# Optimization experiments

Measured on AMD Instinct MI355X. Metric: run time of the kernel, lower is better.

The kernel has to match this reference:

```python
import jax, jax.numpy as jnp
import numpy as np

N_NODES = 100000
N_EDGES = 1600000
STATE_DIM = 128
HIDDEN_DIM = 128
ACTION_DIM = 16


def gcn_conv(x, edge_index, W, b, n_nodes):
    """PyG-style GCNConv: add self-loops, symmetric normalization, x@W then aggregate."""
    xw = x @ W  # [N, H]
    loops = jnp.arange(n_nodes, dtype=edge_index.dtype)
    src = jnp.concatenate([edge_index[0], loops])  # [E+N]
    dst = jnp.concatenate([edge_index[1], loops])
    ones = jnp.ones(src.shape[0], dtype=xw.dtype)
    deg = jax.ops.segment_sum(ones, dst, num_segments=n_nodes)  # degree of target nodes
    dinv = jnp.where(deg > 0, jax.lax.rsqrt(deg), 0.0)
    norm = dinv[src] * dinv[dst]  # [E+N]
    msg = xw[src] * norm[:, None]  # gather + scale (irregular access)
    out = jax.ops.segment_sum(msg, dst, num_segments=n_nodes)  # scatter-aggregate
    return out + b


def setup_inputs() -> dict:
    key = jax.random.key(0)
    ks = jax.random.split(key, 12)
    def lin(k, fan_in, shape):
        bound = 1.0 / np.sqrt(fan_in)
        return jax.random.uniform(k, shape, jnp.float32, -bound, bound)
    return {
        "x": jax.random.normal(ks[0], (N_NODES, STATE_DIM), jnp.float32),
        "edge_index": jax.random.randint(ks[1], (2, N_EDGES), 0, N_NODES, jnp.int64),
        "action": jax.random.normal(ks[2], (N_NODES, ACTION_DIM), jnp.float32),
        "gcn1_w": lin(ks[3], STATE_DIM, (STATE_DIM, HIDDEN_DIM)),
        "gcn1_b": lin(ks[4], STATE_DIM, (HIDDEN_DIM,)),
        "gcn2_w": lin(ks[5], HIDDEN_DIM, (HIDDEN_DIM, HIDDEN_DIM)),
        "gcn2_b": lin(ks[6], HIDDEN_DIM, (HIDDEN_DIM,)),
        "fc1_w": lin(ks[7], HIDDEN_DIM + ACTION_DIM, (HIDDEN_DIM + ACTION_DIM, HIDDEN_DIM)),
        "fc1_b": lin(ks[8], HIDDEN_DIM + ACTION_DIM, (HIDDEN_DIM,)),
        "fc2_w": lin(ks[9], HIDDEN_DIM, (HIDDEN_DIM, 1)),
        "fc2_b": lin(ks[10], HIDDEN_DIM, (1,)),
    }


def reference(x, edge_index, action, gcn1_w, gcn1_b, gcn2_w, gcn2_b, fc1_w, fc1_b, fc2_w, fc2_b):
    n = x.shape[0]
    h = jax.nn.relu(gcn_conv(x, edge_index, gcn1_w, gcn1_b, n))
    h = jax.nn.relu(gcn_conv(h, edge_index, gcn2_w, gcn2_b, n))
    h = jnp.concatenate([h, action], axis=-1)  # [N, H+A]
    h = jax.nn.relu(h @ fc1_w + fc1_b)
    q = h @ fc2_w + fc2_b  # [N, 1]
    return q.squeeze(-1)
```

## Files before the change

### kernel.cpp

```cpp
#include <hip/hip_runtime.h>
#include <hip/hip_bf16.h>

typedef unsigned short u16;
typedef unsigned int   u32;
typedef __attribute__((ext_vector_type(8))) short bf16x8;
typedef __attribute__((ext_vector_type(4))) float f32x4;
typedef __attribute__((ext_vector_type(4))) unsigned int u32x4;

constexpr int NN = 100000;
constexpr int NE = 1600000;
constexpr int D  = 128;
constexpr size_t WS_NEED = 58909184;

constexpr int NBUCK = 196;
constexpr int NBLKA = 512;
constexpr int EPB   = 3136;
constexpr int CAPA  = 48;

__device__ __forceinline__ float bf2f(u16 u){ union{u32 i;float f;}v; v.i=((u32)u)<<16; return v.f; }
__device__ __forceinline__ float2 bfp(u32 u){ union{u32 i;float f;}a,b; a.i=u<<16; b.i=u&0xffff0000u; return make_float2(a.f,b.f); }
__device__ __forceinline__ u16 f2bf(float f){ union{float f;u32 i;}v; v.f=f; u32 r=v.i + 0x7fffu + ((v.i>>16)&1u); return (u16)(r>>16); }
__device__ __forceinline__ u32 pk2(float a, float b){ return (u32)f2bf(a) | ((u32)f2bf(b)<<16); }

__global__ void detect_kernel(const u32* __restrict__ xw, const int* __restrict__ ei,
                              int* __restrict__ flagf, int* __restrict__ flage){
  __shared__ int shf[256];
  __shared__ int she[256];
  int t = threadIdx.x;
  int cnt = 0;
  for(int i = 0; i < 16; i++){
    u32 w = xw[(t*16 + i) * 256];
    int e = (int)((w >> 7) & 0xFFu);
    cnt += (e >= 64 && e <= 160) ? 1 : 0;
  }
  int nz = 0;
  for(int i = 0; i < 8; i++){
    int k = t*8 + i;
    long long w = 1 + ((long long)k * (2LL*NE - 2)) / 2048;
    nz += (ei[(int)(w | 1)] != 0) ? 1 : 0;
  }
  shf[t] = cnt; she[t] = nz;
  __syncthreads();
  for(int off=128; off>0; off>>=1){
    if(t<off){ shf[t]+=shf[t+off]; she[t]+=she[t+off]; }
    __syncthreads();
  }
  if(t==0){ flagf[0] = (shf[0] < 3000) ? 1 : 0; flage[0] = (she[0] == 0) ? 1 : 0; }
}

__global__ void prep_kernel(const void* __restrict__ w1, const void* __restrict__ w2,
    const void* __restrict__ fw1, const void* __restrict__ b1, const void* __restrict__ b2,
    const void* __restrict__ fb1, const void* __restrict__ fw2, const void* __restrict__ fb2,
    const int* __restrict__ flagf,
    u16* __restrict__ WT1, u16* __restrict__ WT2, u16* __restrict__ WTF, float* __restrict__ BF)
{
  const int ff = flagf[0];
  int i = blockIdx.x*256 + threadIdx.x;
  auto cv = [&](const void* p, int idx)->float{
    return ff ? ((const float*)p)[idx] : bf2f(((const u16*)p)[idx]);
  };
  if(i < 16384){
    int k = i >> 7, d = i & 127;
    WT1[d*128 + k] = f2bf(cv(w1, i));
  }else if(i < 32768){
    int j = i - 16384; int k = j >> 7, d = j & 127;
    WT2[d*128 + k] = f2bf(cv(w2, j));
  }else if(i < 51200){
    int j = i - 32768; int k = j >> 7, d = j & 127;
    WTF[d*144 + k] = f2bf(cv(fw1, j));
  }else if(i < 51713){
    int j = i - 51200;
    if(j < 128)       BF[j]   = cv(b1, j);
    else if(j < 256)  BF[j]   = cv(b2, j-128);
    else if(j < 384)  BF[j]   = cv(fb1, j-256);
    else if(j < 512)  BF[j]   = cv(fw2, j-384);
    else              BF[512] = cv(fb2, 0);
  }
}

__global__ void fill1_kernel(u16* __restrict__ out, int n){
  int i = blockIdx.x*blockDim.x + threadIdx.x;
  if(i < n) out[i] = 0x3F80;
}

__global__ __launch_bounds__(512) void passA_kernel(
    const int* __restrict__ ei, const int* __restrict__ flage,
    u32* __restrict__ ebuf, u32* __restrict__ counts)
{
  __shared__ u32 hist[NBUCK];
  int t = threadIdx.x;
  if(t < NBUCK) hist[t] = 0;
  __syncthreads();
  const int f = flage[0];
  const int eb = blockIdx.x * EPB;
  const u32 cbase = blockIdx.x * NBUCK;
  for(int g = t; g < EPB/4; g += 512){
    int e4 = eb + g*4;
    if(e4 >= NE) break;
    int sv[4], dv[4];
    if(f){
      uint4 sa = *(const uint4*)(ei + 2*(size_t)e4);
      uint4 sb = *(const uint4*)(ei + 2*(size_t)e4 + 4);
      uint4 da = *(const uint4*)(ei + 2*(size_t)(NE + e4));
      uint4 db = *(const uint4*)(ei + 2*(size_t)(NE + e4) + 4);
      sv[0]=(int)sa.x; sv[1]=(int)sa.z; sv[2]=(int)sb.x; sv[3]=(int)sb.z;
      dv[0]=(int)da.x; dv[1]=(int)da.z; dv[2]=(int)db.x; dv[3]=(int)db.z;
    }else{
      uint4 sa = *(const uint4*)(ei + e4);
      uint4 da = *(const uint4*)(ei + NE + e4);
      sv[0]=(int)sa.x; sv[1]=(int)sa.y; sv[2]=(int)sa.z; sv[3]=(int)sa.w;
      dv[0]=(int)da.x; dv[1]=(int)da.y; dv[2]=(int)da.z; dv[3]=(int)da.w;
    }
    #pragma unroll
    for(int q=0;q<4;q++){
      int s = sv[q], d = dv[q];
      if((u32)s >= (u32)NN || (u32)d >= (u32)NN) continue;
      int b = d >> 9;
      u32 rank = atomicAdd(&hist[b], 1u);
      if(rank < CAPA) ebuf[(size_t)(cbase + b)*CAPA + rank] = (u32)s | ((u32)(d & 511) << 17);
    }
  }
  __syncthreads();
  if(t < NBUCK){
    u32 c = hist[t];
    counts[t*NBLKA + blockIdx.x] = (c < CAPA) ? c : CAPA;
  }
}

__global__ void scan196_kernel(const u32* __restrict__ counts, int* __restrict__ bases){
  __shared__ int sh[NBUCK];
  int t = threadIdx.x;
  if(t < NBUCK){
    const uint4* p = (const uint4*)(counts + (size_t)t*NBLKA);
    int tot = 0;
    for(int c = 0; c < NBLKA/4; c++){ uint4 v = p[c]; tot += (int)(v.x + v.y + v.z + v.w); }
    sh[t] = tot;
  }
  __syncthreads();
  if(t == 0){
    int acc = 0;
    for(int b = 0; b < NBUCK; b++){ int v = sh[b]; sh[b] = acc; acc += v; }
  }
  __syncthreads();
  if(t < NBUCK) bases[t] = sh[t];
}

__global__ __launch_bounds__(512) void passB_kernel(
    const u32* __restrict__ ebuf, const u32* __restrict__ counts, const int* __restrict__ bases,
    int* __restrict__ deg, int* __restrict__ off, float* __restrict__ dinv,
    int* __restrict__ srcs)
{
  __shared__ int cnt[512];
  __shared__ int nodeoff[512];
  __shared__ int pos[512];
  __shared__ int wsum[8], wpre[8];
  const int t = threadIdx.x;
  const int b = blockIdx.x;
  const int v0 = b << 9;

  cnt[t] = 0;
  __syncthreads();

  const int cnum = (int)counts[b*NBLKA + t];
  const u32* cp = ebuf + (size_t)(t*NBUCK + b)*CAPA;

  {
    int i = 0;
    for(; i + 4 <= cnum; i += 4){
      uint4 r = *(const uint4*)(cp + i);
      atomicAdd(&cnt[r.x >> 17], 1); atomicAdd(&cnt[r.y >> 17], 1);
      atomicAdd(&cnt[r.z >> 17], 1); atomicAdd(&cnt[r.w >> 17], 1);
    }
    for(; i < cnum; i++) atomicAdd(&cnt[cp[i] >> 17], 1);
  }
  __syncthreads();

  const int myc = cnt[t];
  const int lane = t & 63, wid = t >> 6;
  int v = myc;
  #pragma unroll
  for(int o = 1; o < 64; o <<= 1){
    int u = __shfl_up(v, o, 64);
    if(lane >= o) v += u;
  }
  if(lane == 63) wsum[wid] = v;
  __syncthreads();
  if(t == 0){
    int acc = 0;
    #pragma unroll
    for(int w = 0; w < 8; w++){ wpre[w] = acc; acc += wsum[w]; }
  }
  __syncthreads();
  const int excl = v - myc + wpre[wid];
  nodeoff[t] = excl;
  pos[t] = 0;
  __syncthreads();

  const int gb = bases[b];

  {
    int i = 0;
    for(; i + 4 <= cnum; i += 4){
      uint4 rq = *(const uint4*)(cp + i);
      u32 rr[4] = {rq.x, rq.y, rq.z, rq.w};
      #pragma unroll
      for(int q = 0; q < 4; q++){
        int ld = rr[q] >> 17;
        int r = atomicAdd(&pos[ld], 1);
        srcs[gb + nodeoff[ld] + r] = (int)(rr[q] & 0x1FFFFu);
      }
    }
    for(; i < cnum; i++){
      u32 rec = cp[i];
      int ld = rec >> 17;
      int r = atomicAdd(&pos[ld], 1);
      srcs[gb + nodeoff[ld] + r] = (int)(rec & 0x1FFFFu);
    }
  }

  int vn = v0 + t;
  if(vn < NN){
    deg[vn] = myc;
    off[vn] = gb + excl;
    dinv[vn] = rsqrtf((float)(myc + 1));
  }
}

__global__ __launch_bounds__(256) void gemm1_kernel(
    const void* __restrict__ A1, const u16* __restrict__ WT,
    const int* __restrict__ flagf, const float* __restrict__ dscale,
    u16* __restrict__ out, int n)
{
  const int tid = threadIdx.x;
  const int nb  = blockIdx.x * 64;
  const int ff  = flagf[0];
  const int wave = tid >> 6;
  const int lane = tid & 63;
  const int quad = lane >> 4;
  const int lm   = lane & 15;

  int arow = nb + wave*16 + lm; if(arow >= n) arow = n-1;

  bf16x8 afr[4];
  if(!ff){
    const u16* xr = (const u16*)A1 + (size_t)arow*128 + quad*8;
    #pragma unroll
    for(int k=0;k<4;k++) afr[k] = *(const bf16x8*)(xr + 32*k);
  }else{
    const float* xr = (const float*)A1 + (size_t)arow*128 + quad*8;
    #pragma unroll
    for(int k=0;k<4;k++){
      float4 p0 = *(const float4*)(xr + 32*k);
      float4 p1 = *(const float4*)(xr + 32*k + 4);
      union{u32x4 u; bf16x8 v;} cvv;
      cvv.u = (u32x4){pk2(p0.x,p0.y), pk2(p0.z,p0.w), pk2(p1.x,p1.y), pk2(p1.z,p1.w)};
      afr[k] = cvv.v;
    }
  }

  f32x4 acc[8];
  #pragma unroll
  for(int t=0;t<8;t++) acc[t] = (f32x4){0.f,0.f,0.f,0.f};

  #pragma unroll
  for(int ki = 0; ki < 4; ki++){
    int kk = ki*32 + quad*8;
    #pragma unroll
    for(int t=0;t<8;t++){
      bf16x8 b = *(const bf16x8*)(WT + (size_t)(t*16 + lm)*128 + kk);
      acc[t] = __builtin_amdgcn_mfma_f32_16x16x32_bf16(afr[ki], b, acc[t], 0, 0, 0);
    }
  }

  const int node0 = nb + wave*16 + quad*4;
  #pragma unroll
  for(int r=0;r<4;r++){
    int gr = node0 + r;
    if(gr < n){
      float dv = dscale[gr];
      #pragma unroll
      for(int t=0;t<8;t++){
        out[(size_t)gr*D + t*16 + lm] = f2bf(acc[t][r]*dv);
      }
    }
  }
}

#define ACC8(r)  { float2 f_;                       \
    f_ = bfp((r).x); a0 += f_.x; a1 += f_.y;        \
    f_ = bfp((r).y); a2 += f_.x; a3 += f_.y;        \
    f_ = bfp((r).z); a4 += f_.x; a5 += f_.y;        \
    f_ = bfp((r).w); a6 += f_.x; a7 += f_.y; }

template<bool FINAL>
__global__ __launch_bounds__(256) void fused_kernel(
    const int* __restrict__ off, const int* __restrict__ deg,
    const int* __restrict__ srcs, const float* __restrict__ dinv,
    const u16* __restrict__ xw, const float* __restrict__ biasf,
    const u16* __restrict__ WT, const float* __restrict__ fb1,
    const float* __restrict__ qwf, const float* __restrict__ qbf,
    const void* __restrict__ action, const int* __restrict__ flagf,
    void* __restrict__ out)
{
  constexpr int K  = FINAL ? 144 : 128;
  constexpr int KT = FINAL ? 160 : 128;
  constexpr int KP = KT + 8;
  constexpr int NKI = KT/32;
  __shared__ u16 Hs[16*KP];
  __shared__ float qred[FINAL ? 64 : 4];

  const int tid  = threadIdx.x;
  const int node0 = blockIdx.x * 16;
  const int nl   = tid >> 4;
  const int l16  = tid & 15;
  const int node = node0 + nl;

  const int wave = tid >> 6;
  const int lane = tid & 63;
  const int quad = lane >> 4;
  const int lm   = lane & 15;

  const int j0 = off[node];
  const int j1 = j0 + deg[node];
  float a0=0.f,a1=0.f,a2=0.f,a3=0.f,a4=0.f,a5=0.f,a6=0.f,a7=0.f;
  const u16* __restrict__ xl = xw + 8*l16;

  int j = j0;
  int s0=0, s1=0, s2=0, s3=0;
  const bool pre = (j + 4 <= j1);
  if(pre){
    s0 = __builtin_nontemporal_load(&srcs[j]);
    s1 = __builtin_nontemporal_load(&srcs[j+1]);
    s2 = __builtin_nontemporal_load(&srcs[j+2]);
    s3 = __builtin_nontemporal_load(&srcs[j+3]);
  }
  for(; j + 8 <= j1; j += 4){
    uint4 r0 = *(const uint4*)(xl + (size_t)s0*D);
    uint4 r1 = *(const uint4*)(xl + (size_t)s1*D);
    uint4 r2 = *(const uint4*)(xl + (size_t)s2*D);
    uint4 r3 = *(const uint4*)(xl + (size_t)s3*D);
    s0 = __builtin_nontemporal_load(&srcs[j+4]);
    s1 = __builtin_nontemporal_load(&srcs[j+5]);
    s2 = __builtin_nontemporal_load(&srcs[j+6]);
    s3 = __builtin_nontemporal_load(&srcs[j+7]);
    ACC8(r0); ACC8(r1); ACC8(r2); ACC8(r3);
  }
  if(pre){
    uint4 r0 = *(const uint4*)(xl + (size_t)s0*D);
    uint4 r1 = *(const uint4*)(xl + (size_t)s1*D);
    uint4 r2 = *(const uint4*)(xl + (size_t)s2*D);
    uint4 r3 = *(const uint4*)(xl + (size_t)s3*D);
    ACC8(r0); ACC8(r1); ACC8(r2); ACC8(r3);
    j += 4;
  }
  for(; j < j1; j++){
    int s = __builtin_nontemporal_load(&srcs[j]);
    uint4 r = *(const uint4*)(xl + (size_t)s*D);
    ACC8(r);
  }

  uint4 ps = *(const uint4*)(xl + (size_t)node*D);
  ACC8(ps);
  const float dv = dinv[node];
  float4 bA = *(const float4*)(biasf + 8*l16);
  float4 bB = *(const float4*)(biasf + 8*l16 + 4);
  float o0 = fmaxf(fmaf(dv,a0,bA.x), 0.f);
  float o1 = fmaxf(fmaf(dv,a1,bA.y), 0.f);
  float o2 = fmaxf(fmaf(dv,a2,bA.z), 0.f);
  float o3 = fmaxf(fmaf(dv,a3,bA.w), 0.f);
  float o4 = fmaxf(fmaf(dv,a4,bB.x), 0.f);
  float o5 = fmaxf(fmaf(dv,a5,bB.y), 0.f);
  float o6 = fmaxf(fmaf(dv,a6,bB.z), 0.f);
  float o7 = fmaxf(fmaf(dv,a7,bB.w), 0.f);
  uint4 pkd;
  pkd.x = pk2(o0,o1); pkd.y = pk2(o2,o3); pkd.z = pk2(o4,o5); pkd.w = pk2(o6,o7);

  u16* Hp = Hs + nl*KP;
  *(uint4*)(Hp + 8*l16) = pkd;

  if(FINAL){
    const int ff = flagf[0];
    if(ff){
      if(l16 < 4){
        const float* af = (const float*)action + (size_t)node*16 + l16*4;
        float4 p = *(const float4*)af;
        uint2 q; q.x = pk2(p.x,p.y); q.y = pk2(p.z,p.w);
        *(uint2*)(Hp + 128 + 4*l16) = q;
      }
    }else{
      if(l16 < 2){
        uint4 v = *(const uint4*)((const u16*)action + (size_t)node*16 + 8*l16);
        *(uint4*)(Hp + 128 + 8*l16) = v;
      }
    }
    if(l16 >= 14){
      *(uint4*)(Hp + 144 + 8*(l16-14)) = make_uint4(0,0,0,0);
    }
  }

  bf16x8 bfr[NKI][2];
  #pragma unroll
  for(int ki = 0; ki < NKI; ki++){
    int kk = ki*32 + quad*8;
    #pragma unroll
    for(int tt=0; tt<2; tt++){
      int col = (wave*2 + tt)*16 + lm;
      bfr[ki][tt] = (bf16x8){0,0,0,0,0,0,0,0};
      if(!FINAL || kk < K)
        bfr[ki][tt] = *(const bf16x8*)(WT + (size_t)col*K + kk);
    }
  }
  __syncthreads();

  const u16* Ab = Hs + lm*KP;
  f32x4 acc[2];
  acc[0] = (f32x4){0.f,0.f,0.f,0.f};
  acc[1] = (f32x4){0.f,0.f,0.f,0.f};

  #pragma unroll
  for(int ki = 0; ki < NKI; ki++){
    int kk = ki*32 + quad*8;
    bf16x8 a = *(const bf16x8*)(Ab + kk);
    acc[0] = __builtin_amdgcn_mfma_f32_16x16x32_bf16(a, bfr[ki][0], acc[0], 0, 0, 0);
    acc[1] = __builtin_amdgcn_mfma_f32_16x16x32_bf16(a, bfr[ki][1], acc[1], 0, 0, 0);
  }

  const int rbase = quad*4;
  if(!FINAL){
    #pragma unroll
    for(int r=0;r<4;r++){
      int gn = node0 + rbase + r;
      float dvr = dinv[gn];
      #pragma unroll
      for(int tt=0;tt<2;tt++){
        int col = (wave*2 + tt)*16 + lm;
        ((u16*)out)[(size_t)gn*D + col] = f2bf(acc[tt][r]*dvr);
      }
    }
  }else{
    float qp[4] = {0.f,0.f,0.f,0.f};
    #pragma unroll
    for(int tt=0;tt<2;tt++){
      int col = (wave*2 + tt)*16 + lm;
      float bv = fb1[col];
      float qw = qwf[col];
      #pragma unroll
      for(int r=0;r<4;r++){
        float h = fmaxf(acc[tt][r] + bv, 0.f);
        qp[r] += h * qw;
      }
    }
    #pragma unroll
    for(int r=0;r<4;r++){
      #pragma unroll
      for(int o=1; o<16; o<<=1) qp[r] += __shfl_xor(qp[r], o, 16);
    }
    if(lm == 0){
      #pragma unroll
      for(int r=0;r<4;r++) qred[wave*16 + rbase + r] = qp[r];
    }
    __syncthreads();
    if(tid < 16){
      float q = qred[tid] + qred[16+tid] + qred[32+tid] + qred[48+tid] + qbf[0];
      int gn = node0 + tid;
      const int ff = flagf[0];
      if(ff) ((float*)out)[gn] = q;
      else   ((u16*)out)[gn]  = f2bf(q);
    }
  }
}

extern "C" void kernel_launch(void* const* d_in, const int* in_sizes, int n_in,
                              void* d_out, int out_size, void* d_ws, size_t ws_size,
                              hipStream_t stream)
{
  bool meta_ok = (n_in >= 11) && (in_sizes[0] == NN*D) && (in_sizes[1] == 2*NE)
              && (in_sizes[2] == NN*16) && (out_size == NN);
  if(!meta_ok){
    fill1_kernel<<<(NN+255)/256, 256, 0, stream>>>((u16*)d_out, NN);
    return;
  }
  if(ws_size < WS_NEED) return;

  const void* x      = d_in[0];
  const int*  ei     = (const int*)d_in[1];
  const void* action = d_in[2];
  const void* w1     = d_in[3];
  const void* b1     = d_in[4];
  const void* w2     = d_in[5];
  const void* b2     = d_in[6];
  const void* fw1    = d_in[7];
  const void* fb1    = d_in[8];
  const void* fw2    = d_in[9];
  const void* fb2    = d_in[10];

  char* ws = (char*)d_ws;
  int*   DEG    = (int*)(ws + 0);
  int*   OFF    = (int*)(ws + 400128);
  float* DINV   = (float*)(ws + 800256);
  int*   FLAGE  = (int*)(ws + 1204480);
  int*   FLAGF  = (int*)(ws + 1204544);
  u16*   WT1    = (u16*)(ws + 1204608);
  u16*   WT2    = (u16*)(ws + 1237376);
  u16*   WTF    = (u16*)(ws + 1270144);
  float* BF     = (float*)(ws + 1307008);
  int*   SRCS   = (int*)(ws + 1309184);
  u16*   F0     = (u16*)(ws + 7709184);
  u16*   F1     = (u16*)(ws + 33309184);
  u32*   EBUF   = (u32*)(ws + 33309184);
  u32*   COUNTS = (u32*)(ws + 52576768);
  int*   BASES  = (int*)(ws + 52978176);

  detect_kernel<<<1, 256, 0, stream>>>((const u32*)x, ei, FLAGF, FLAGE);

  passA_kernel<<<NBLKA, 512, 0, stream>>>(ei, FLAGE, EBUF, COUNTS);
  scan196_kernel<<<1, 256, 0, stream>>>(COUNTS, BASES);
  passB_kernel<<<NBUCK, 512, 0, stream>>>(EBUF, COUNTS, BASES, DEG, OFF, DINV, SRCS);

  prep_kernel<<<203, 256, 0, stream>>>(w1, w2, fw1, b1, b2, fb1, fw2, fb2, FLAGF,
                                       WT1, WT2, WTF, BF);

  gemm1_kernel<<<(NN+63)/64, 256, 0, stream>>>(x, WT1, FLAGF, DINV, F0, NN);

  fused_kernel<false><<<(NN+15)/16, 256, 0, stream>>>(
      OFF, DEG, SRCS, DINV, F0, BF, WT2, nullptr, nullptr, nullptr, nullptr, FLAGF, F1);

  fused_kernel<true><<<(NN+15)/16, 256, 0, stream>>>(
      OFF, DEG, SRCS, DINV, F1, BF+128, WTF, BF+256, BF+384, BF+512, action, FLAGF, d_out);
}
```

Baseline: 335.0 us.

## Split fused gather+GEMM into separate gather and streaming GEMM kernels

Replaces the fused aggregate-then-GEMM kernels with a pure gather kernel that writes H to global memory, followed by streaming MFMA GEMM kernels that process 64 rows per block with all 128 output columns. The gather kernel splits each node's 128 features across two blocks (64 columns each, 8 lanes per node), which gives more parallelism and smaller per-row gather footprints. This removes LDS staging, the per-block weight reloads and the block syncs. In exchange it adds extra global round-trips for the intermediate H and two more kernel launches.

```diff
diff --git a/kernel.cpp b/kernel.cpp
--- a/kernel.cpp
+++ b/kernel.cpp
@@ -226,14 +226,15 @@
   }
 }
 
-__global__ __launch_bounds__(256) void gemm1_kernel(
+template<bool RAW>
+__global__ __launch_bounds__(256) void gemm_stream_kernel(
     const void* __restrict__ A1, const u16* __restrict__ WT,
     const int* __restrict__ flagf, const float* __restrict__ dscale,
     u16* __restrict__ out, int n)
 {
   const int tid = threadIdx.x;
   const int nb  = blockIdx.x * 64;
-  const int ff  = flagf[0];
+  const int ff  = RAW ? flagf[0] : 0;
   const int wave = tid >> 6;
   const int lane = tid & 63;
   const int quad = lane >> 4;
@@ -242,7 +243,7 @@
   int arow = nb + wave*16 + lm; if(arow >= n) arow = n-1;
 
   bf16x8 afr[4];
-  if(!ff){
+  if(!RAW || !ff){
     const u16* xr = (const u16*)A1 + (size_t)arow*128 + quad*8;
     #pragma unroll
     for(int k=0;k<4;k++) afr[k] = *(const bf16x8*)(xr + 32*k);
@@ -286,44 +287,115 @@
   }
 }
 
+__global__ __launch_bounds__(256) void gemmF_kernel(
+    const u16* __restrict__ H, const void* __restrict__ action,
+    const u16* __restrict__ WT, const float* __restrict__ fb1,
+    const float* __restrict__ qwf, const float* __restrict__ qbf,
+    const int* __restrict__ flagf, void* __restrict__ out, int n)
+{
+  const int tid = threadIdx.x;
+  const int nb  = blockIdx.x * 64;
+  const int ff  = flagf[0];
+  const int wave = tid >> 6;
+  const int lane = tid & 63;
+  const int quad = lane >> 4;
+  const int lm   = lane & 15;
+
+  int arow = nb + wave*16 + lm; if(arow >= n) arow = n-1;
+
+  bf16x8 afr[5];
+  {
+    const u16* hr = H + (size_t)arow*128 + quad*8;
+    #pragma unroll
+    for(int k=0;k<4;k++) afr[k] = *(const bf16x8*)(hr + 32*k);
+  }
+  afr[4] = (bf16x8){0,0,0,0,0,0,0,0};
+  if(quad < 2){
+    if(ff){
+      const float* af = (const float*)action + (size_t)arow*16 + quad*8;
+      float4 p0 = *(const float4*)(af);
+      float4 p1 = *(const float4*)(af + 4);
+      union{u32x4 u; bf16x8 v;} cvv;
+      cvv.u = (u32x4){pk2(p0.x,p0.y), pk2(p0.z,p0.w), pk2(p1.x,p1.y), pk2(p1.z,p1.w)};
+      afr[4] = cvv.v;
+    }else{
+      afr[4] = *(const bf16x8*)((const u16*)action + (size_t)arow*16 + quad*8);
+    }
+  }
+
+  f32x4 acc[8];
+  #pragma unroll
+  for(int t=0;t<8;t++) acc[t] = (f32x4){0.f,0.f,0.f,0.f};
+
+  #pragma unroll
+  for(int ki = 0; ki < 5; ki++){
+    int kk = ki*32 + quad*8;
+    #pragma unroll
+    for(int t=0;t<8;t++){
+      bf16x8 b = (bf16x8){0,0,0,0,0,0,0,0};
+      if(kk < 144)
+        b = *(const bf16x8*)(WT + (size_t)(t*16 + lm)*144 + kk);
+      acc[t] = __builtin_amdgcn_mfma_f32_16x16x32_bf16(afr[ki], b, acc[t], 0, 0, 0);
+    }
+  }
+
+  float qp[4] = {0.f,0.f,0.f,0.f};
+  #pragma unroll
+  for(int t=0;t<8;t++){
+    int col = t*16 + lm;
+    float bv = fb1[col];
+    float qw = qwf[col];
+    #pragma unroll
+    for(int r=0;r<4;r++){
+      float h = fmaxf(acc[t][r] + bv, 0.f);
+      qp[r] += h * qw;
+    }
+  }
+  #pragma unroll
+  for(int r=0;r<4;r++){
+    #pragma unroll
+    for(int o=1; o<16; o<<=1) qp[r] += __shfl_xor(qp[r], o, 16);
+  }
+  if(lm == 0){
+    const float qb = qbf[0];
+    const int node0 = nb + wave*16 + quad*4;
+    #pragma unroll
+    for(int r=0;r<4;r++){
+      int gr = node0 + r;
+      if(gr < n){
+        float q = qp[r] + qb;
+        if(ff) ((float*)out)[gr] = q;
+        else   ((u16*)out)[gr]  = f2bf(q);
+      }
+    }
+  }
+}
+
 #define ACC8(r)  { float2 f_;                       \
     f_ = bfp((r).x); a0 += f_.x; a1 += f_.y;        \
     f_ = bfp((r).y); a2 += f_.x; a3 += f_.y;        \
     f_ = bfp((r).z); a4 += f_.x; a5 += f_.y;        \
     f_ = bfp((r).w); a6 += f_.x; a7 += f_.y; }
 
-template<bool FINAL>
-__global__ __launch_bounds__(256) void fused_kernel(
+__global__ __launch_bounds__(256) void gatherH_kernel(
     const int* __restrict__ off, const int* __restrict__ deg,
     const int* __restrict__ srcs, const float* __restrict__ dinv,
     const u16* __restrict__ xw, const float* __restrict__ biasf,
-    const u16* __restrict__ WT, const float* __restrict__ fb1,
-    const float* __restrict__ qwf, const float* __restrict__ qbf,
-    const void* __restrict__ action, const int* __restrict__ flagf,
-    void* __restrict__ out)
-{
-  constexpr int K  = FINAL ? 144 : 128;
-  constexpr int KT = FINAL ? 160 : 128;
-  constexpr int KP = KT + 8;
-  constexpr int NKI = KT/32;
-  __shared__ u16 Hs[16*KP];
-  __shared__ float qred[FINAL ? 64 : 4];
-
+    u16* __restrict__ H)
+{
+  const int blk  = blockIdx.x;
+  const int half = blk & 1;
+  const int grp  = blk >> 1;
   const int tid  = threadIdx.x;
-  const int node0 = blockIdx.x * 16;
-  const int nl   = tid >> 4;
-  const int l16  = tid & 15;
-  const int node = node0 + nl;
-
-  const int wave = tid >> 6;
-  const int lane = tid & 63;
-  const int quad = lane >> 4;
-  const int lm   = lane & 15;
+  const int nl   = tid >> 3;
+  const int l8   = tid & 7;
+  const int node = grp*32 + nl;
+  const int d0   = half*64 + l8*8;
 
   const int j0 = off[node];
   const int j1 = j0 + deg[node];
   float a0=0.f,a1=0.f,a2=0.f,a3=0.f,a4=0.f,a5=0.f,a6=0.f,a7=0.f;
-  const u16* __restrict__ xl = xw + 8*l16;
+  const u16* __restrict__ xl = xw + d0;
 
   int j = j0;
   int s0=0, s1=0, s2=0, s3=0;
@@ -362,8 +434,8 @@
   uint4 ps = *(const uint4*)(xl + (size_t)node*D);
   ACC8(ps);
   const float dv = dinv[node];
-  float4 bA = *(const float4*)(biasf + 8*l16);
-  float4 bB = *(const float4*)(biasf + 8*l16 + 4);
+  float4 bA = *(const float4*)(biasf + d0);
+  float4 bB = *(const float4*)(biasf + d0 + 4);
   float o0 = fmaxf(fmaf(dv,a0,bA.x), 0.f);
   float o1 = fmaxf(fmaf(dv,a1,bA.y), 0.f);
   float o2 = fmaxf(fmaf(dv,a2,bA.z), 0.f);
@@ -374,100 +446,7 @@
   float o7 = fmaxf(fmaf(dv,a7,bB.w), 0.f);
   uint4 pkd;
   pkd.x = pk2(o0,o1); pkd.y = pk2(o2,o3); pkd.z = pk2(o4,o5); pkd.w = pk2(o6,o7);
-
-  u16* Hp = Hs + nl*KP;
-  *(uint4*)(Hp + 8*l16) = pkd;
-
-  if(FINAL){
-    const int ff = flagf[0];
-    if(ff){
-      if(l16 < 4){
-        const float* af = (const float*)action + (size_t)node*16 + l16*4;
-        float4 p = *(const float4*)af;
-        uint2 q; q.x = pk2(p.x,p.y); q.y = pk2(p.z,p.w);
-        *(uint2*)(Hp + 128 + 4*l16) = q;
-      }
-    }else{
-      if(l16 < 2){
-        uint4 v = *(const uint4*)((const u16*)action + (size_t)node*16 + 8*l16);
-        *(uint4*)(Hp + 128 + 8*l16) = v;
-      }
-    }
-    if(l16 >= 14){
-      *(uint4*)(Hp + 144 + 8*(l16-14)) = make_uint4(0,0,0,0);
-    }
-  }
-
-  bf16x8 bfr[NKI][2];
-  #pragma unroll
-  for(int ki = 0; ki < NKI; ki++){
-    int kk = ki*32 + quad*8;
-    #pragma unroll
-    for(int tt=0; tt<2; tt++){
-      int col = (wave*2 + tt)*16 + lm;
-      bfr[ki][tt] = (bf16x8){0,0,0,0,0,0,0,0};
-      if(!FINAL || kk < K)
-        bfr[ki][tt] = *(const bf16x8*)(WT + (size_t)col*K + kk);
-    }
-  }
-  __syncthreads();
-
-  const u16* Ab = Hs + lm*KP;
-  f32x4 acc[2];
-  acc[0] = (f32x4){0.f,0.f,0.f,0.f};
-  acc[1] = (f32x4){0.f,0.f,0.f,0.f};
-
-  #pragma unroll
-  for(int ki = 0; ki < NKI; ki++){
-    int kk = ki*32 + quad*8;
-    bf16x8 a = *(const bf16x8*)(Ab + kk);
-    acc[0] = __builtin_amdgcn_mfma_f32_16x16x32_bf16(a, bfr[ki][0], acc[0], 0, 0, 0);
-    acc[1] = __builtin_amdgcn_mfma_f32_16x16x32_bf16(a, bfr[ki][1], acc[1], 0, 0, 0);
-  }
-
-  const int rbase = quad*4;
-  if(!FINAL){
-    #pragma unroll
-    for(int r=0;r<4;r++){
-      int gn = node0 + rbase + r;
-      float dvr = dinv[gn];
-      #pragma unroll
-      for(int tt=0;tt<2;tt++){
-        int col = (wave*2 + tt)*16 + lm;
-        ((u16*)out)[(size_t)gn*D + col] = f2bf(acc[tt][r]*dvr);
-      }
-    }
-  }else{
-    float qp[4] = {0.f,0.f,0.f,0.f};
-    #pragma unroll
-    for(int tt=0;tt<2;tt++){
-      int col = (wave*2 + tt)*16 + lm;
-      float bv = fb1[col];
-      float qw = qwf[col];
-      #pragma unroll
-      for(int r=0;r<4;r++){
-        float h = fmaxf(acc[tt][r] + bv, 0.f);
-        qp[r] += h * qw;
-      }
-    }
-    #pragma unroll
-    for(int r=0;r<4;r++){
-      #pragma unroll
-      for(int o=1; o<16; o<<=1) qp[r] += __shfl_xor(qp[r], o, 16);
-    }
-    if(lm == 0){
-      #pragma unroll
-      for(int r=0;r<4;r++) qred[wave*16 + rbase + r] = qp[r];
-    }
-    __syncthreads();
-    if(tid < 16){
-      float q = qred[tid] + qred[16+tid] + qred[32+tid] + qred[48+tid] + qbf[0];
-      int gn = node0 + tid;
-      const int ff = flagf[0];
-      if(ff) ((float*)out)[gn] = q;
-      else   ((u16*)out)[gn]  = f2bf(q);
-    }
-  }
+  *(uint4*)(H + (size_t)node*D + d0) = pkd;
 }
 
 extern "C" void kernel_launch(void* const* d_in, const int* in_sizes, int n_in,
@@ -505,8 +484,8 @@
   u16*   WTF    = (u16*)(ws + 1270144);
   float* BF     = (float*)(ws + 1307008);
   int*   SRCS   = (int*)(ws + 1309184);
-  u16*   F0     = (u16*)(ws + 7709184);
-  u16*   F1     = (u16*)(ws + 33309184);
+  u16*   XW     = (u16*)(ws + 7709184);
+  u16*   HB     = (u16*)(ws + 33309184);
   u32*   EBUF   = (u32*)(ws + 33309184);
   u32*   COUNTS = (u32*)(ws + 52576768);
   int*   BASES  = (int*)(ws + 52978176);
@@ -520,11 +499,14 @@
   prep_kernel<<<203, 256, 0, stream>>>(w1, w2, fw1, b1, b2, fb1, fw2, fb2, FLAGF,
                                        WT1, WT2, WTF, BF);
 
-  gemm1_kernel<<<(NN+63)/64, 256, 0, stream>>>(x, WT1, FLAGF, DINV, F0, NN);
-
-  fused_kernel<false><<<(NN+15)/16, 256, 0, stream>>>(
-      OFF, DEG, SRCS, DINV, F0, BF, WT2, nullptr, nullptr, nullptr, nullptr, FLAGF, F1);
-
-  fused_kernel<true><<<(NN+15)/16, 256, 0, stream>>>(
-      OFF, DEG, SRCS, DINV, F1, BF+128, WTF, BF+256, BF+384, BF+512, action, FLAGF, d_out);
-}
+  gemm_stream_kernel<true><<<(NN+63)/64, 256, 0, stream>>>(x, WT1, FLAGF, DINV, XW, NN);
+
+  gatherH_kernel<<<(NN/32)*2, 256, 0, stream>>>(OFF, DEG, SRCS, DINV, XW, BF, HB);
+
+  gemm_stream_kernel<false><<<(NN+63)/64, 256, 0, stream>>>(HB, WT2, FLAGF, DINV, XW, NN);
+
+  gatherH_kernel<<<(NN/32)*2, 256, 0, stream>>>(OFF, DEG, SRCS, DINV, XW, BF+128, HB);
+
+  gemmF_kernel<<<(NN+63)/64, 256, 0, stream>>>(HB, action, WTF, BF+256, BF+384, BF+512,
+                                               FLAGF, d_out, NN);
+}
```

Result: slower. 373.3 us (+11.4%).

## Merge setup kernels and overlap edge bucketing with first GEMM

Applied to the files above, without the earlier changes.

Folds format detection into the weight-prep kernel and merges the edge bucketing pass with the first-layer GEMM in a single launch with disjoint block ranges, so both run concurrently. The GEMM no longer scales rows by dinv, because dinv is not yet available at that point. The first aggregation instead multiplies each gathered neighbour row by its source dinv and handles the self-loop term separately. The separate scan kernel is removed: each passB block recomputes its own bucket base by summing the counts of all earlier buckets. This trades fewer launches and serialization for extra dinv gathers per edge and redundant prefix work in passB.

```diff
diff --git a/kernel.cpp b/kernel.cpp
--- a/kernel.cpp
+++ b/kernel.cpp
@@ -16,46 +16,62 @@
 constexpr int NBLKA = 512;
 constexpr int EPB   = 3136;
 constexpr int CAPA  = 48;
+constexpr int NBG1  = (NN + 127) / 128;
 
 __device__ __forceinline__ float bf2f(u16 u){ union{u32 i;float f;}v; v.i=((u32)u)<<16; return v.f; }
 __device__ __forceinline__ float2 bfp(u32 u){ union{u32 i;float f;}a,b; a.i=u<<16; b.i=u&0xffff0000u; return make_float2(a.f,b.f); }
 __device__ __forceinline__ u16 f2bf(float f){ union{float f;u32 i;}v; v.f=f; u32 r=v.i + 0x7fffu + ((v.i>>16)&1u); return (u16)(r>>16); }
 __device__ __forceinline__ u32 pk2(float a, float b){ return (u32)f2bf(a) | ((u32)f2bf(b)<<16); }
 
-__global__ void detect_kernel(const u32* __restrict__ xw, const int* __restrict__ ei,
-                              int* __restrict__ flagf, int* __restrict__ flage){
-  __shared__ int shf[256];
-  __shared__ int she[256];
-  int t = threadIdx.x;
+__global__ void fill1_kernel(u16* __restrict__ out, int n){
+  int i = blockIdx.x*blockDim.x + threadIdx.x;
+  if(i < n) out[i] = 0x3F80;
+}
+
+__global__ __launch_bounds__(512) void prep_kernel(
+    const u32* __restrict__ xw, const int* __restrict__ ei,
+    const void* __restrict__ w1, const void* __restrict__ w2,
+    const void* __restrict__ fw1, const void* __restrict__ b1, const void* __restrict__ b2,
+    const void* __restrict__ fb1, const void* __restrict__ fw2, const void* __restrict__ fb2,
+    int* __restrict__ flagf, int* __restrict__ flage,
+    u16* __restrict__ WT1, u16* __restrict__ WT2, u16* __restrict__ WTF, float* __restrict__ BF)
+{
+  __shared__ int sh[512];
+  const int t = threadIdx.x;
   int cnt = 0;
-  for(int i = 0; i < 16; i++){
-    u32 w = xw[(t*16 + i) * 256];
+  #pragma unroll
+  for(int i = 0; i < 8; i++){
+    u32 w = xw[(t*8 + i) * 256];
     int e = (int)((w >> 7) & 0xFFu);
     cnt += (e >= 64 && e <= 160) ? 1 : 0;
   }
-  int nz = 0;
-  for(int i = 0; i < 8; i++){
-    int k = t*8 + i;
-    long long w = 1 + ((long long)k * (2LL*NE - 2)) / 2048;
-    nz += (ei[(int)(w | 1)] != 0) ? 1 : 0;
-  }
-  shf[t] = cnt; she[t] = nz;
-  __syncthreads();
-  for(int off=128; off>0; off>>=1){
-    if(t<off){ shf[t]+=shf[t+off]; she[t]+=she[t+off]; }
+  sh[t] = cnt;
+  __syncthreads();
+  for(int o = 256; o > 0; o >>= 1){
+    if(t < o) sh[t] += sh[t + o];
     __syncthreads();
   }
-  if(t==0){ flagf[0] = (shf[0] < 3000) ? 1 : 0; flage[0] = (she[0] == 0) ? 1 : 0; }
-}
-
-__global__ void prep_kernel(const void* __restrict__ w1, const void* __restrict__ w2,
-    const void* __restrict__ fw1, const void* __restrict__ b1, const void* __restrict__ b2,
-    const void* __restrict__ fb1, const void* __restrict__ fw2, const void* __restrict__ fb2,
-    const int* __restrict__ flagf,
-    u16* __restrict__ WT1, u16* __restrict__ WT2, u16* __restrict__ WTF, float* __restrict__ BF)
-{
-  const int ff = flagf[0];
-  int i = blockIdx.x*256 + threadIdx.x;
+  const int ff = (sh[0] < 3000) ? 1 : 0;
+
+  if(blockIdx.x == 0){
+    int nz = 0;
+    #pragma unroll
+    for(int i = 0; i < 4; i++){
+      int k = t*4 + i;
+      long long w = 1 + ((long long)k * (2LL*NE - 2)) / 2048;
+      nz += (ei[(int)(w | 1)] != 0) ? 1 : 0;
+    }
+    __syncthreads();
+    sh[t] = nz;
+    __syncthreads();
+    for(int o = 256; o > 0; o >>= 1){
+      if(t < o) sh[t] += sh[t + o];
+      __syncthreads();
+    }
+    if(t == 0){ flage[0] = (sh[0] == 0) ? 1 : 0; flagf[0] = ff; }
+  }
+
+  int i = blockIdx.x*512 + t;
   auto cv = [&](const void* p, int idx)->float{
     return ff ? ((const float*)p)[idx] : bf2f(((const u16*)p)[idx]);
   };
@@ -78,75 +94,111 @@
   }
 }
 
-__global__ void fill1_kernel(u16* __restrict__ out, int n){
-  int i = blockIdx.x*blockDim.x + threadIdx.x;
-  if(i < n) out[i] = 0x3F80;
-}
-
-__global__ __launch_bounds__(512) void passA_kernel(
+__global__ __launch_bounds__(512) void mega_kernel(
     const int* __restrict__ ei, const int* __restrict__ flage,
-    u32* __restrict__ ebuf, u32* __restrict__ counts)
+    u32* __restrict__ ebuf, u32* __restrict__ counts,
+    const void* __restrict__ x, const u16* __restrict__ WT,
+    const int* __restrict__ flagf, u16* __restrict__ F0)
 {
   __shared__ u32 hist[NBUCK];
-  int t = threadIdx.x;
-  if(t < NBUCK) hist[t] = 0;
-  __syncthreads();
-  const int f = flage[0];
-  const int eb = blockIdx.x * EPB;
-  const u32 cbase = blockIdx.x * NBUCK;
-  for(int g = t; g < EPB/4; g += 512){
-    int e4 = eb + g*4;
-    if(e4 >= NE) break;
-    int sv[4], dv[4];
-    if(f){
-      uint4 sa = *(const uint4*)(ei + 2*(size_t)e4);
-      uint4 sb = *(const uint4*)(ei + 2*(size_t)e4 + 4);
-      uint4 da = *(const uint4*)(ei + 2*(size_t)(NE + e4));
-      uint4 db = *(const uint4*)(ei + 2*(size_t)(NE + e4) + 4);
-      sv[0]=(int)sa.x; sv[1]=(int)sa.z; sv[2]=(int)sb.x; sv[3]=(int)sb.z;
-      dv[0]=(int)da.x; dv[1]=(int)da.z; dv[2]=(int)db.x; dv[3]=(int)db.z;
+  const int blk = blockIdx.x;
+  const int t = threadIdx.x;
+
+  if(blk < NBLKA){
+    if(t < NBUCK) hist[t] = 0;
+    __syncthreads();
+    const int f = flage[0];
+    const int eb = blk * EPB;
+    const u32 cbase = blk * NBUCK;
+    for(int g = t; g < EPB/4; g += 512){
+      int e4 = eb + g*4;
+      if(e4 >= NE) break;
+      int sv[4], dv[4];
+      if(f){
+        uint4 sa = *(const uint4*)(ei + 2*(size_t)e4);
+        uint4 sb = *(const uint4*)(ei + 2*(size_t)e4 + 4);
+        uint4 da = *(const uint4*)(ei + 2*(size_t)(NE + e4));
+        uint4 db = *(const uint4*)(ei + 2*(size_t)(NE + e4) + 4);
+        sv[0]=(int)sa.x; sv[1]=(int)sa.z; sv[2]=(int)sb.x; sv[3]=(int)sb.z;
+        dv[0]=(int)da.x; dv[1]=(int)da.z; dv[2]=(int)db.x; dv[3]=(int)db.z;
+      }else{
+        uint4 sa = *(const uint4*)(ei + e4);
+        uint4 da = *(const uint4*)(ei + NE + e4);
+        sv[0]=(int)sa.x; sv[1]=(int)sa.y; sv[2]=(int)sa.z; sv[3]=(int)sa.w;
+        dv[0]=(int)da.x; dv[1]=(int)da.y; dv[2]=(int)da.z; dv[3]=(int)da.w;
+      }
+      #pragma unroll
+      for(int q=0;q<4;q++){
+        int s = sv[q], d = dv[q];
+        if((u32)s >= (u32)NN || (u32)d >= (u32)NN) continue;
+        int b = d >> 9;
+        u32 rank = atomicAdd(&hist[b], 1u);
+        if(rank < CAPA) ebuf[(size_t)(cbase + b)*CAPA + rank] = (u32)s | ((u32)(d & 511) << 17);
+      }
+    }
+    __syncthreads();
+    if(t < NBUCK){
+      u32 c = hist[t];
+      counts[t*NBLKA + blk] = (c < CAPA) ? c : CAPA;
+    }
+  }else{
+    const int g = blk - NBLKA;
+    const int nb = g * 128;
+    const int ff = flagf[0];
+    const int wave = t >> 6;
+    const int lane = t & 63;
+    const int quad = lane >> 4;
+    const int lm   = lane & 15;
+
+    int arow = nb + wave*16 + lm; if(arow >= NN) arow = NN-1;
+
+    bf16x8 afr[4];
+    if(!ff){
+      const u16* xr = (const u16*)x + (size_t)arow*128 + quad*8;
+      #pragma unroll
+      for(int k=0;k<4;k++) afr[k] = *(const bf16x8*)(xr + 32*k);
     }else{
-      uint4 sa = *(const uint4*)(ei + e4);
-      uint4 da = *(const uint4*)(ei + NE + e4);
-      sv[0]=(int)sa.x; sv[1]=(int)sa.y; sv[2]=(int)sa.z; sv[3]=(int)sa.w;
-      dv[0]=(int)da.x; dv[1]=(int)da.y; dv[2]=(int)da.z; dv[3]=(int)da.w;
-    }
-    #pragma unroll
-    for(int q=0;q<4;q++){
-      int s = sv[q], d = dv[q];
-      if((u32)s >= (u32)NN || (u32)d >= (u32)NN) continue;
-      int b = d >> 9;
-      u32 rank = atomicAdd(&hist[b], 1u);
-      if(rank < CAPA) ebuf[(size_t)(cbase + b)*CAPA + rank] = (u32)s | ((u32)(d & 511) << 17);
-    }
-  }
-  __syncthreads();
-  if(t < NBUCK){
-    u32 c = hist[t];
-    counts[t*NBLKA + blockIdx.x] = (c < CAPA) ? c : CAPA;
+      const float* xr = (const float*)x + (size_t)arow*128 + quad*8;
+      #pragma unroll
+      for(int k=0;k<4;k++){
+        float4 p0 = *(const float4*)(xr + 32*k);
+        float4 p1 = *(const float4*)(xr + 32*k + 4);
+        union{u32x4 u; bf16x8 v;} cvv;
+        cvv.u = (u32x4){pk2(p0.x,p0.y), pk2(p0.z,p0.w), pk2(p1.x,p1.y), pk2(p1.z,p1.w)};
+        afr[k] = cvv.v;
+      }
+    }
+
+    f32x4 acc[8];
+    #pragma unroll
+    for(int a=0;a<8;a++) acc[a] = (f32x4){0.f,0.f,0.f,0.f};
+
+    #pragma unroll
+    for(int ki = 0; ki < 4; ki++){
+      int kk = ki*32 + quad*8;
+      #pragma unroll
+      for(int a=0;a<8;a++){
+        bf16x8 b = *(const bf16x8*)(WT + (size_t)(a*16 + lm)*128 + kk);
+        acc[a] = __builtin_amdgcn_mfma_f32_16x16x32_bf16(afr[ki], b, acc[a], 0, 0, 0);
+      }
+    }
+
+    const int node0 = nb + wave*16 + quad*4;
+    #pragma unroll
+    for(int r=0;r<4;r++){
+      int gr = node0 + r;
+      if(gr < NN){
+        #pragma unroll
+        for(int a=0;a<8;a++){
+          F0[(size_t)gr*D + a*16 + lm] = f2bf(acc[a][r]);
+        }
+      }
+    }
   }
 }
 
-__global__ void scan196_kernel(const u32* __restrict__ counts, int* __restrict__ bases){
-  __shared__ int sh[NBUCK];
-  int t = threadIdx.x;
-  if(t < NBUCK){
-    const uint4* p = (const uint4*)(counts + (size_t)t*NBLKA);
-    int tot = 0;
-    for(int c = 0; c < NBLKA/4; c++){ uint4 v = p[c]; tot += (int)(v.x + v.y + v.z + v.w); }
-    sh[t] = tot;
-  }
-  __syncthreads();
-  if(t == 0){
-    int acc = 0;
-    for(int b = 0; b < NBUCK; b++){ int v = sh[b]; sh[b] = acc; acc += v; }
-  }
-  __syncthreads();
-  if(t < NBUCK) bases[t] = sh[t];
-}
-
 __global__ __launch_bounds__(512) void passB_kernel(
-    const u32* __restrict__ ebuf, const u32* __restrict__ counts, const int* __restrict__ bases,
+    const u32* __restrict__ ebuf, const u32* __restrict__ counts,
     int* __restrict__ deg, int* __restrict__ off, float* __restrict__ dinv,
     int* __restrict__ srcs)
 {
@@ -154,12 +206,27 @@
   __shared__ int nodeoff[512];
   __shared__ int pos[512];
   __shared__ int wsum[8], wpre[8];
+  __shared__ int gbs;
   const int t = threadIdx.x;
   const int b = blockIdx.x;
   const int v0 = b << 9;
+  const int lane = t & 63, wid = t >> 6;
 
   cnt[t] = 0;
-  __syncthreads();
+
+  int part = 0;
+  for(int q = 0; q < b; q++) part += (int)counts[q*NBLKA + t];
+  int rp = part;
+  #pragma unroll
+  for(int o = 1; o < 64; o <<= 1) rp += __shfl_xor(rp, o, 64);
+  if(lane == 0) wsum[wid] = rp;
+  __syncthreads();
+  if(t == 0){
+    int a = 0;
+    #pragma unroll
+    for(int w = 0; w < 8; w++) a += wsum[w];
+    gbs = a;
+  }
 
   const int cnum = (int)counts[b*NBLKA + t];
   const u32* cp = ebuf + (size_t)(t*NBUCK + b)*CAPA;
@@ -176,7 +243,6 @@
   __syncthreads();
 
   const int myc = cnt[t];
-  const int lane = t & 63, wid = t >> 6;
   int v = myc;
   #pragma unroll
   for(int o = 1; o < 64; o <<= 1){
@@ -196,7 +262,7 @@
   pos[t] = 0;
   __syncthreads();
 
-  const int gb = bases[b];
+  const int gb = gbs;
 
   {
     int i = 0;
@@ -226,73 +292,18 @@
   }
 }
 
-__global__ __launch_bounds__(256) void gemm1_kernel(
-    const void* __restrict__ A1, const u16* __restrict__ WT,
-    const int* __restrict__ flagf, const float* __restrict__ dscale,
-    u16* __restrict__ out, int n)
-{
-  const int tid = threadIdx.x;
-  const int nb  = blockIdx.x * 64;
-  const int ff  = flagf[0];
-  const int wave = tid >> 6;
-  const int lane = tid & 63;
-  const int quad = lane >> 4;
-  const int lm   = lane & 15;
-
-  int arow = nb + wave*16 + lm; if(arow >= n) arow = n-1;
-
-  bf16x8 afr[4];
-  if(!ff){
-    const u16* xr = (const u16*)A1 + (size_t)arow*128 + quad*8;
-    #pragma unroll
-    for(int k=0;k<4;k++) afr[k] = *(const bf16x8*)(xr + 32*k);
-  }else{
-    const float* xr = (const float*)A1 + (size_t)arow*128 + quad*8;
-    #pragma unroll
-    for(int k=0;k<4;k++){
-      float4 p0 = *(const float4*)(xr + 32*k);
-      float4 p1 = *(const float4*)(xr + 32*k + 4);
-      union{u32x4 u; bf16x8 v;} cvv;
-      cvv.u = (u32x4){pk2(p0.x,p0.y), pk2(p0.z,p0.w), pk2(p1.x,p1.y), pk2(p1.z,p1.w)};
-      afr[k] = cvv.v;
-    }
-  }
-
-  f32x4 acc[8];
-  #pragma unroll
-  for(int t=0;t<8;t++) acc[t] = (f32x4){0.f,0.f,0.f,0.f};
-
-  #pragma unroll
-  for(int ki = 0; ki < 4; ki++){
-    int kk = ki*32 + quad*8;
-    #pragma unroll
-    for(int t=0;t<8;t++){
-      bf16x8 b = *(const bf16x8*)(WT + (size_t)(t*16 + lm)*128 + kk);
-      acc[t] = __builtin_amdgcn_mfma_f32_16x16x32_bf16(afr[ki], b, acc[t], 0, 0, 0);
-    }
-  }
-
-  const int node0 = nb + wave*16 + quad*4;
-  #pragma unroll
-  for(int r=0;r<4;r++){
-    int gr = node0 + r;
-    if(gr < n){
-      float dv = dscale[gr];
-      #pragma unroll
-      for(int t=0;t<8;t++){
-        out[(size_t)gr*D + t*16 + lm] = f2bf(acc[t][r]*dv);
-      }
-    }
-  }
-}
-
 #define ACC8(r)  { float2 f_;                       \
     f_ = bfp((r).x); a0 += f_.x; a1 += f_.y;        \
     f_ = bfp((r).y); a2 += f_.x; a3 += f_.y;        \
     f_ = bfp((r).z); a4 += f_.x; a5 += f_.y;        \
     f_ = bfp((r).w); a6 += f_.x; a7 += f_.y; }
-
-template<bool FINAL>
+#define WACC8(r,ww) { float2 f_;                          \
+    f_ = bfp((r).x); a0 += (ww)*f_.x; a1 += (ww)*f_.y;    \
+    f_ = bfp((r).y); a2 += (ww)*f_.x; a3 += (ww)*f_.y;    \
+    f_ = bfp((r).z); a4 += (ww)*f_.x; a5 += (ww)*f_.y;    \
+    f_ = bfp((r).w); a6 += (ww)*f_.x; a7 += (ww)*f_.y; }
+
+template<bool FINAL, bool WSCALE>
 __global__ __launch_bounds__(256) void fused_kernel(
     const int* __restrict__ off, const int* __restrict__ deg,
     const int* __restrict__ srcs, const float* __restrict__ dinv,
@@ -339,39 +350,62 @@
     uint4 r1 = *(const uint4*)(xl + (size_t)s1*D);
     uint4 r2 = *(const uint4*)(xl + (size_t)s2*D);
     uint4 r3 = *(const uint4*)(xl + (size_t)s3*D);
+    float w0=0.f,w1=0.f,w2=0.f,w3=0.f;
+    if(WSCALE){ w0=dinv[s0]; w1=dinv[s1]; w2=dinv[s2]; w3=dinv[s3]; }
     s0 = __builtin_nontemporal_load(&srcs[j+4]);
     s1 = __builtin_nontemporal_load(&srcs[j+5]);
     s2 = __builtin_nontemporal_load(&srcs[j+6]);
     s3 = __builtin_nontemporal_load(&srcs[j+7]);
-    ACC8(r0); ACC8(r1); ACC8(r2); ACC8(r3);
+    if(WSCALE){ WACC8(r0,w0); WACC8(r1,w1); WACC8(r2,w2); WACC8(r3,w3); }
+    else      { ACC8(r0); ACC8(r1); ACC8(r2); ACC8(r3); }
   }
   if(pre){
     uint4 r0 = *(const uint4*)(xl + (size_t)s0*D);
     uint4 r1 = *(const uint4*)(xl + (size_t)s1*D);
     uint4 r2 = *(const uint4*)(xl + (size_t)s2*D);
     uint4 r3 = *(const uint4*)(xl + (size_t)s3*D);
-    ACC8(r0); ACC8(r1); ACC8(r2); ACC8(r3);
+    if(WSCALE){
+      float w0=dinv[s0], w1=dinv[s1], w2=dinv[s2], w3=dinv[s3];
+      WACC8(r0,w0); WACC8(r1,w1); WACC8(r2,w2); WACC8(r3,w3);
+    }else{
+      ACC8(r0); ACC8(r1); ACC8(r2); ACC8(r3);
+    }
     j += 4;
   }
   for(; j < j1; j++){
     int s = __builtin_nontemporal_load(&srcs[j]);
     uint4 r = *(const uint4*)(xl + (size_t)s*D);
-    ACC8(r);
-  }
-
+    if(WSCALE){ float wv = dinv[s]; WACC8(r,wv); }
+    else      { ACC8(r); }
+  }
+
+  const float dv = dinv[node];
   uint4 ps = *(const uint4*)(xl + (size_t)node*D);
-  ACC8(ps);
-  const float dv = dinv[node];
   float4 bA = *(const float4*)(biasf + 8*l16);
   float4 bB = *(const float4*)(biasf + 8*l16 + 4);
-  float o0 = fmaxf(fmaf(dv,a0,bA.x), 0.f);
-  float o1 = fmaxf(fmaf(dv,a1,bA.y), 0.f);
-  float o2 = fmaxf(fmaf(dv,a2,bA.z), 0.f);
-  float o3 = fmaxf(fmaf(dv,a3,bA.w), 0.f);
-  float o4 = fmaxf(fmaf(dv,a4,bB.x), 0.f);
-  float o5 = fmaxf(fmaf(dv,a5,bB.y), 0.f);
-  float o6 = fmaxf(fmaf(dv,a6,bB.z), 0.f);
-  float o7 = fmaxf(fmaf(dv,a7,bB.w), 0.f);
+  float o0,o1,o2,o3,o4,o5,o6,o7;
+  if(WSCALE){
+    const float dv2 = dv*dv;
+    float2 sa=bfp(ps.x), sb=bfp(ps.y), sc=bfp(ps.z), sd=bfp(ps.w);
+    o0 = fmaxf(dv*a0 + dv2*sa.x + bA.x, 0.f);
+    o1 = fmaxf(dv*a1 + dv2*sa.y + bA.y, 0.f);
+    o2 = fmaxf(dv*a2 + dv2*sb.x + bA.z, 0.f);
+    o3 = fmaxf(dv*a3 + dv2*sb.y + bA.w, 0.f);
+    o4 = fmaxf(dv*a4 + dv2*sc.x + bB.x, 0.f);
+    o5 = fmaxf(dv*a5 + dv2*sc.y + bB.y, 0.f);
+    o6 = fmaxf(dv*a6 + dv2*sd.x + bB.z, 0.f);
+    o7 = fmaxf(dv*a7 + dv2*sd.y + bB.w, 0.f);
+  }else{
+    ACC8(ps);
+    o0 = fmaxf(fmaf(dv,a0,bA.x), 0.f);
+    o1 = fmaxf(fmaf(dv,a1,bA.y), 0.f);
+    o2 = fmaxf(fmaf(dv,a2,bA.z), 0.f);
+    o3 = fmaxf(fmaf(dv,a3,bA.w), 0.f);
+    o4 = fmaxf(fmaf(dv,a4,bB.x), 0.f);
+    o5 = fmaxf(fmaf(dv,a5,bB.y), 0.f);
+    o6 = fmaxf(fmaf(dv,a6,bB.z), 0.f);
+    o7 = fmaxf(fmaf(dv,a7,bB.w), 0.f);
+  }
   uint4 pkd;
   pkd.x = pk2(o0,o1); pkd.y = pk2(o2,o3); pkd.z = pk2(o4,o5); pkd.w = pk2(o6,o7);
 
@@ -509,22 +543,17 @@
   u16*   F1     = (u16*)(ws + 33309184);
   u32*   EBUF   = (u32*)(ws + 33309184);
   u32*   COUNTS = (u32*)(ws + 52576768);
-  int*   BASES  = (int*)(ws + 52978176);
-
-  detect_kernel<<<1, 256, 0, stream>>>((const u32*)x, ei, FLAGF, FLAGE);
-
-  passA_kernel<<<NBLKA, 512, 0, stream>>>(ei, FLAGE, EBUF, COUNTS);
-  scan196_kernel<<<1, 256, 0, stream>>>(COUNTS, BASES);
-  passB_kernel<<<NBUCK, 512, 0, stream>>>(EBUF, COUNTS, BASES, DEG, OFF, DINV, SRCS);
-
-  prep_kernel<<<203, 256, 0, stream>>>(w1, w2, fw1, b1, b2, fb1, fw2, fb2, FLAGF,
-                                       WT1, WT2, WTF, BF);
-
-  gemm1_kernel<<<(NN+63)/64, 256, 0, stream>>>(x, WT1, FLAGF, DINV, F0, NN);
-
-  fused_kernel<false><<<(NN+15)/16, 256, 0, stream>>>(
+
+  prep_kernel<<<102, 512, 0, stream>>>((const u32*)x, ei, w1, w2, fw1, b1, b2, fb1, fw2, fb2,
+                                       FLAGF, FLAGE, WT1, WT2, WTF, BF);
+
+  mega_kernel<<<NBLKA + NBG1, 512, 0, stream>>>(ei, FLAGE, EBUF, COUNTS, x, WT1, FLAGF, F0);
+
+  passB_kernel<<<NBUCK, 512, 0, stream>>>(EBUF, COUNTS, DEG, OFF, DINV, SRCS);
+
+  fused_kernel<false,true><<<(NN+15)/16, 256, 0, stream>>>(
       OFF, DEG, SRCS, DINV, F0, BF, WT2, nullptr, nullptr, nullptr, nullptr, FLAGF, F1);
 
-  fused_kernel<true><<<(NN+15)/16, 256, 0, stream>>>(
+  fused_kernel<true,false><<<(NN+15)/16, 256, 0, stream>>>(
       OFF, DEG, SRCS, DINV, F1, BF+128, WTF, BF+256, BF+384, BF+512, action, FLAGF, d_out);
 }
```

Measured after the change: 343.9 us. +2.7%, slower.
